# Kernel optimization log

Measured on AMD Instinct MI355X. Metric: run time of the kernel, lower is better.

The kernel has to match this reference:

```python
import jax, jax.numpy as jnp
import numpy as np

B, C, D, H, W = 4096, 64, 4, 4, 4
E, DIM = 16384, 4096  # num_embeddings, embedding_dim = C*D*H*W
COMMITMENT_COST = 0.25


def setup_inputs() -> dict:
    key = jax.random.key(0)
    k1, k2 = jax.random.split(key)
    inputs = jax.random.normal(k1, (B, C, D, H, W), dtype=jnp.float32)
    limit = 1.0 / E
    embed_w = jax.random.uniform(k2, (E, DIM), dtype=jnp.float32,
                                 minval=-limit, maxval=limit)
    return {"inputs": inputs, "embed_w": embed_w}


def reference(inputs, embed_w):
    sg = jax.lax.stop_gradient
    input_shape = inputs.shape
    flat = inputs.reshape(inputs.shape[0], -1)  # [B, DIM]
    distances = (jnp.sum(flat * flat, axis=1, keepdims=True)
                 + jnp.sum(embed_w * embed_w, axis=1)
                 - 2.0 * jnp.matmul(flat, embed_w.T))
    encoding_indices = jnp.argmin(distances, axis=1)  # [B]
    encodings = jax.nn.one_hot(encoding_indices, E, dtype=jnp.float32)  # [B, E]
    # gather nearest codebook vectors (same math as one_hot @ embed_w)
    quantized = embed_w[encoding_indices].reshape(input_shape)
    e_latent_loss = jnp.mean((sg(quantized) - inputs) ** 2)
    q_latent_loss = jnp.mean((quantized - sg(inputs)) ** 2)
    loss = q_latent_loss + COMMITMENT_COST * e_latent_loss
    # straight-through estimator
    quantized = inputs + sg(quantized - inputs)
    avg_probs = jnp.mean(encodings, axis=0)  # [E]
    perplexity = jnp.exp(-jnp.sum(avg_probs * jnp.log(avg_probs + 1e-10)))
    return loss, quantized, perplexity, encodings
```

## Files before the change

kernel.cpp:

```cpp
#include <hip/hip_runtime.h>

typedef unsigned long long u64;
typedef unsigned int u32;
typedef unsigned short u16;

typedef __attribute__((ext_vector_type(8))) short short8;
typedef __attribute__((ext_vector_type(4))) short short4v;
typedef __attribute__((ext_vector_type(4))) float floatx4;

static constexpr int BROWS = 4096;
static constexpr int ENUM_ = 16384;
static constexpr int KD    = 4096;
static constexpr int CANDMAX = 65536;
#define MARGIN 4e-4f


__device__ __forceinline__ u32 sortable(float d) {
  u32 u = __float_as_uint(d);
  return (u & 0x80000000u) ? ~u : (u | 0x80000000u);
}
__device__ __forceinline__ float unsortable(u32 k) {
  u32 u = (k & 0x80000000u) ? (k & 0x7fffffffu) : ~k;
  return __uint_as_float(u);
}

__device__ __forceinline__ u16 f2bf_rn(float f) {
  u32 u = __float_as_uint(f);
  u32 r = (u + 0x7fffu + ((u >> 16) & 1u)) >> 16;
  return (u16)r;
}
__device__ __forceinline__ float bf2f(u16 h) {
  return __uint_as_float((u32)h << 16);
}

__device__ __forceinline__ void gload_lds16(const void* g, void* l) {
  __builtin_amdgcn_global_load_lds((const __attribute__((address_space(1))) void*)g,
                                   (__attribute__((address_space(3))) void*)l,
                                   16, 0, 0);
}

__device__ __forceinline__ float blockReduceSumF(float v) {
  __shared__ float s[4];
  #pragma unroll
  for (int o = 32; o > 0; o >>= 1) v += __shfl_down(v, o);
  int lane = threadIdx.x & 63, wid = threadIdx.x >> 6;
  if (lane == 0) s[wid] = v;
  __syncthreads();
  float r = 0.f;
  if (threadIdx.x == 0) r = s[0] + s[1] + s[2] + s[3];
  return r;
}

__device__ __forceinline__ double blockReduceSumD(double v) {
  __shared__ double s[4];
  #pragma unroll
  for (int o = 32; o > 0; o >>= 1) v += __shfl_down(v, o);
  int lane = threadIdx.x & 63, wid = threadIdx.x >> 6;
  if (lane == 0) s[wid] = v;
  __syncthreads();
  double r = 0.0;
  if (threadIdx.x == 0) r = s[0] + s[1] + s[2] + s[3];
  return r;
}


__global__ __launch_bounds__(256) void split_hi(const float* __restrict__ src,
                                                u16* __restrict__ hi, int n8) {
  int t = blockIdx.x * 256 + threadIdx.x;
  if (t >= n8) return;
  const float4* s = (const float4*)src + (size_t)t * 2;
  float4 a = s[0], b = s[1];
  float v[8] = {a.x, a.y, a.z, a.w, b.x, b.y, b.z, b.w};
  short h[8];
  #pragma unroll
  for (int i = 0; i < 8; ++i) h[i] = (short)f2bf_rn(v[i]);
  *(short8*)(hi + (size_t)t * 8) = *(short8*)h;
}

__global__ __launch_bounds__(256) void split_w_e2(const float* __restrict__ w,
                                                  u16* __restrict__ hi,
                                                  float* __restrict__ e2) {
  int j = blockIdx.x;
  const float4* wr = (const float4*)(w + (size_t)j * KD);
  u16* hr = hi + (size_t)j * KD;
  float local = 0.f;
  #pragma unroll
  for (int t = 0; t < 4; ++t) {
    int e = threadIdx.x + t * 256;
    float4 v = wr[e];
    local += v.x * v.x + v.y * v.y + v.z * v.z + v.w * v.w;
    short h[4] = {(short)f2bf_rn(v.x), (short)f2bf_rn(v.y),
                  (short)f2bf_rn(v.z), (short)f2bf_rn(v.w)};
    *(short4v*)(hr + (size_t)e * 4) = *(short4v*)h;
  }
  float tot = blockReduceSumF(local);
  if (threadIdx.x == 0) e2[j] = tot;
}

__global__ __launch_bounds__(256) void split_kernel(const float* __restrict__ src,
                                                    u16* __restrict__ hi,
                                                    u16* __restrict__ lo, int n8) {
  int t = blockIdx.x * 256 + threadIdx.x;
  if (t >= n8) return;
  const float4* s = (const float4*)src + (size_t)t * 2;
  float4 a = s[0], b = s[1];
  float v[8] = {a.x, a.y, a.z, a.w, b.x, b.y, b.z, b.w};
  short h[8], l[8];
  #pragma unroll
  for (int i = 0; i < 8; ++i) {
    u16 hh = f2bf_rn(v[i]);
    h[i] = (short)hh;
    l[i] = (short)f2bf_rn(v[i] - bf2f(hh));
  }
  *(short8*)(hi + (size_t)t * 8) = *(short8*)h;
  *(short8*)(lo + (size_t)t * 8) = *(short8*)l;
}

__global__ __launch_bounds__(256) void e2_kernel(const float* __restrict__ w,
                                                 float* __restrict__ e2) {
  int j = blockIdx.x;
  const float4* wr = (const float4*)(w + (size_t)j * KD);
  float local = 0.f;
  #pragma unroll
  for (int t = 0; t < 4; ++t) {
    float4 v = wr[threadIdx.x + t * 256];
    local += v.x * v.x + v.y * v.y + v.z * v.z + v.w * v.w;
  }
  float tot = blockReduceSumF(local);
  if (threadIdx.x == 0) e2[j] = tot;
}

__global__ __launch_bounds__(512, 2)
void gemm_hi8(const u16* __restrict__ Ah, const u16* __restrict__ Bh,
              const float* __restrict__ e2, u16* __restrict__ dist,
              u64* __restrict__ best) {
  __shared__ char smem[131072];
  constexpr int NT = KD / 64;

  const u32 wg = blockIdx.x;
  const u32 swz = (wg & 7) * 128 + (wg >> 3);
  const int by = swz & 15;
  const int bx = swz >> 4;
  const int row0 = by * 256, col0 = bx * 256;

  const int t = threadIdx.x;
  const int lane = t & 63, wv = t >> 6;
  const int wr = wv >> 2, wc = wv & 3;
  const int quad = lane >> 4, lcol = lane & 15;

  const int m0 = t >> 2;
  const int g0 = (t & 3) ^ ((t >> 3) & 3);
  const size_t aG0 = (size_t)(row0 + m0) * KD + g0 * 8;
  const size_t bG0 = (size_t)(col0 + m0) * KD + g0 * 8;
  const size_t rowStep = (size_t)128 * KD;

  auto stage = [&](int tau, int k) {
    if (tau >= NT) return;
    char* base = smem + (tau & 1) * 65536 +
                 (k == 0 ? 0 : (k == 1 ? 32768 : (k == 2 ? 16384 : 49152)));
    size_t gofs = ((k == 0 || k == 2) ? aG0 : bG0) +
                  (size_t)tau * 64 + (k >= 2 ? 32 : 0);
    const u16* src = (k == 0 || k == 2) ? Ah : Bh;
    gload_lds16(src + gofs, base + t * 16);
    gload_lds16(src + gofs + rowStep, base + t * 16 + 8192);
  };

  stage(0, 0); stage(0, 1); stage(0, 2); stage(0, 3);
  stage(1, 0); stage(1, 1);
  asm volatile("s_waitcnt vmcnt(4)" ::: "memory");
  asm volatile("s_barrier" ::: "memory");

  floatx4 acc[8][4] = {};

  for (int tt = 0; tt < NT; ++tt) {
    char* buf = smem + (tt & 1) * 65536;
    short8 bf[4];
    #pragma unroll
    for (int c = 0; c < 4; ++c) {
      const int ks = c >> 1, mh = c & 1;
      const char* Ar = buf + ks * 16384;
      const char* Br = buf + 32768 + ks * 16384;

      short8 af[4];
      #pragma unroll
      for (int r = 0; r < 4; ++r) {
        int m = wr * 128 + mh * 64 + r * 16 + lcol;
        af[r] = *(const short8*)(Ar + m * 64 + ((quad ^ ((m >> 1) & 3)) << 4));
      }
      if (mh == 0) {
        #pragma unroll
        for (int n = 0; n < 4; ++n) {
          int mm = wc * 64 + n * 16 + lcol;
          bf[n] = *(const short8*)(Br + mm * 64 + ((quad ^ ((mm >> 1) & 3)) << 4));
        }
      }

      if (c == 0)      stage(tt + 1, 2);
      else if (c == 1) stage(tt + 1, 3);
      else if (c == 2) stage(tt + 2, 0);
      else             stage(tt + 2, 1);

      asm volatile("s_barrier" ::: "memory");
      __builtin_amdgcn_s_setprio(1);
      #pragma unroll
      for (int r = 0; r < 4; ++r)
        #pragma unroll
        for (int n = 0; n < 4; ++n)
          acc[mh * 4 + r][n] = __builtin_amdgcn_mfma_f32_16x16x32_bf16(
              af[r], bf[n], acc[mh * 4 + r][n], 0, 0, 0);
      __builtin_amdgcn_s_setprio(0);
      if (c == 3) asm volatile("s_waitcnt vmcnt(4)" ::: "memory");
      asm volatile("s_barrier" ::: "memory");
    }
  }

  float e2v[4];
  #pragma unroll
  for (int n = 0; n < 4; ++n) e2v[n] = e2[col0 + wc * 64 + n * 16 + lcol];

  #pragma unroll
  for (int fm = 0; fm < 8; ++fm) {
    #pragma unroll
    for (int i = 0; i < 4; ++i) {
      int grow = row0 + wr * 128 + fm * 16 + quad * 4 + i;
      u64 kmin = ~0ull;
      #pragma unroll
      for (int n = 0; n < 4; ++n) {
        int gcol = col0 + wc * 64 + n * 16 + lcol;
        float d = __fadd_rn(e2v[n], __fmul_rn(-2.0f, acc[fm][n][i]));
        dist[(size_t)grow * ENUM_ + gcol] = f2bf_rn(d);
        u64 key = ((u64)sortable(d) << 32) | (u32)gcol;
        kmin = key < kmin ? key : kmin;
      }
      #pragma unroll
      for (int msk = 1; msk < 16; msk <<= 1) {
        u64 o = __shfl_xor(kmin, msk);
        kmin = o < kmin ? o : kmin;
      }
      if (lcol == 0) atomicMin(&best[grow], kmin);
    }
  }
}

__global__ __launch_bounds__(256)
void scan_kernel(const u16* __restrict__ dist, const u64* __restrict__ best,
                 u64* __restrict__ cand, int* __restrict__ ccount) {
  const int n8 = BROWS * ENUM_ / 8;
  int step = gridDim.x * 256;
  for (int f = blockIdx.x * 256 + threadIdx.x; f < n8; f += step) {
    int i = f >> 11;
    float limit = unsortable((u32)(best[i] >> 32)) + MARGIN;
    short8 v = ((const short8*)dist)[f];
    #pragma unroll
    for (int e = 0; e < 8; ++e) {
      float d = bf2f((u16)v[e]);
      if (d <= limit) {
        int pos = atomicAdd(ccount, 1);
        if (pos < CANDMAX) cand[pos] = ((u64)(u32)i << 32) | (u32)(f * 8 + e - i * ENUM_);
      }
    }
  }
}

__global__ __launch_bounds__(256)
void refine_kernel(const float* __restrict__ x, const float* __restrict__ w,
                   const u64* __restrict__ cand, const int* __restrict__ ccount,
                   u64* __restrict__ best2) {
  int cnt = *ccount;
  if (cnt > CANDMAX) cnt = CANDMAX;
  for (int b = blockIdx.x; b < cnt; b += gridDim.x) {
    u64 cd = cand[b];
    int i = (int)(cd >> 32), j = (int)(cd & 0xffffffffu);
    const float4* xr = (const float4*)(x + (size_t)i * KD);
    const float4* wr = (const float4*)(w + (size_t)j * KD);
    double local = 0.0;
    #pragma unroll
    for (int t = 0; t < 4; ++t) {
      int e = threadIdx.x + t * 256;
      float4 xv = xr[e], wv = wr[e];
      local += (double)wv.x * ((double)wv.x - 2.0 * (double)xv.x)
             + (double)wv.y * ((double)wv.y - 2.0 * (double)xv.y)
             + (double)wv.z * ((double)wv.z - 2.0 * (double)xv.z)
             + (double)wv.w * ((double)wv.w - 2.0 * (double)xv.w);
    }
    double d = blockReduceSumD(local);
    if (threadIdx.x == 0) {
      u64 key = ((u64)sortable((float)d) << 32) | (u32)j;
      atomicMin(&best2[i], key);
    }
    __syncthreads();
  }
}

__global__ __launch_bounds__(256)
void gemm_argmin_mfma(const u16* __restrict__ Ah, const u16* __restrict__ Al,
                      const u16* __restrict__ Bh, const u16* __restrict__ Bl,
                      const float* __restrict__ e2, u64* __restrict__ best) {
  __shared__ char smem[32768];
  const int by = blockIdx.x, bx = blockIdx.y;
  const int row0 = by * 128, col0 = bx * 128;
  const int t = threadIdx.x;
  const int lane = t & 63, wv = t >> 6;
  const int wr = wv >> 1, wc = wv & 1;
  const int srow = t >> 2;
  const int schunk = (t & 3) ^ ((t >> 3) & 3);
  const size_t aoff0 = (size_t)(row0 + srow) * KD + schunk * 8;
  const size_t aoff1 = aoff0 + (size_t)64 * KD;
  const size_t boff0 = (size_t)(col0 + srow) * KD + schunk * 8;
  const size_t boff1 = boff0 + (size_t)64 * KD;
  char* sAh = smem; char* sAl = smem + 8192;
  char* sBh = smem + 16384; char* sBl = smem + 24576;
  const int d0 = t * 16, d1 = 4096 + t * 16;
  floatx4 acc[4][4] = {};
  for (int kk = 0; kk < KD; kk += 32) {
    __syncthreads();
    gload_lds16(Ah + aoff0 + kk, sAh + d0);
    gload_lds16(Ah + aoff1 + kk, sAh + d1);
    gload_lds16(Al + aoff0 + kk, sAl + d0);
    gload_lds16(Al + aoff1 + kk, sAl + d1);
    gload_lds16(Bh + boff0 + kk, sBh + d0);
    gload_lds16(Bh + boff1 + kk, sBh + d1);
    gload_lds16(Bl + boff0 + kk, sBl + d0);
    gload_lds16(Bl + boff1 + kk, sBl + d1);
    __syncthreads();
    short8 afh[4], afl[4];
    #pragma unroll
    for (int r = 0; r < 4; ++r) {
      int m = wr * 64 + r * 16 + (lane & 15);
      int off = m * 64 + (((lane >> 4) ^ ((m >> 1) & 3)) * 16);
      afh[r] = *(const short8*)(sAh + off);
      afl[r] = *(const short8*)(sAl + off);
    }
    #pragma unroll
    for (int c = 0; c < 4; ++c) {
      int m = wc * 64 + c * 16 + (lane & 15);
      int off = m * 64 + (((lane >> 4) ^ ((m >> 1) & 3)) * 16);
      short8 bfh = *(const short8*)(sBh + off);
      short8 bfl = *(const short8*)(sBl + off);
      #pragma unroll
      for (int r = 0; r < 4; ++r) {
        acc[r][c] = __builtin_amdgcn_mfma_f32_16x16x32_bf16(afh[r], bfh, acc[r][c], 0, 0, 0);
        acc[r][c] = __builtin_amdgcn_mfma_f32_16x16x32_bf16(afl[r], bfh, acc[r][c], 0, 0, 0);
        acc[r][c] = __builtin_amdgcn_mfma_f32_16x16x32_bf16(afh[r], bfl, acc[r][c], 0, 0, 0);
      }
    }
  }
  const int quad = lane >> 4, lcol = lane & 15;
  float e2v[4];
  #pragma unroll
  for (int c = 0; c < 4; ++c) e2v[c] = e2[col0 + wc * 64 + c * 16 + lcol];
  #pragma unroll
  for (int r = 0; r < 4; ++r) {
    #pragma unroll
    for (int i = 0; i < 4; ++i) {
      int grow = row0 + wr * 64 + r * 16 + quad * 4 + i;
      u64 kmin = ~0ull;
      #pragma unroll
      for (int c = 0; c < 4; ++c) {
        int gcol = col0 + wc * 64 + c * 16 + lcol;
        float d = __fadd_rn(e2v[c], __fmul_rn(-2.0f, acc[r][c][i]));
        u64 key = ((u64)sortable(d) << 32) | (u32)gcol;
        kmin = key < kmin ? key : kmin;
      }
      #pragma unroll
      for (int msk = 1; msk < 16; msk <<= 1) {
        u64 o = __shfl_xor(kmin, msk);
        kmin = o < kmin ? o : kmin;
      }
      if (lcol == 0) atomicMin(&best[grow], kmin);
    }
  }
}

__global__ __launch_bounds__(256)
void gemm_argmin(const float* __restrict__ A, const float* __restrict__ W,
                 const float* __restrict__ e2, u64* __restrict__ best) {
  __shared__ union {
    struct { float As[8][128]; float Bs[8][128]; } st;
    u64 red[128 * 16];
  } sm;
  const int by = blockIdx.x, bx = blockIdx.y;
  const int tid = threadIdx.x;
  const int tx = tid & 15, ty = tid >> 4;
  const int row0 = by * 128, col0 = bx * 128;
  const int lm = tid >> 1, lk = (tid & 1) * 4;
  const float* Ap = A + (size_t)(row0 + lm) * KD + lk;
  const float* Wp = W + (size_t)(col0 + lm) * KD + lk;
  float acc[8][8];
  #pragma unroll
  for (int r = 0; r < 8; ++r)
    #pragma unroll
    for (int c = 0; c < 8; ++c) acc[r][c] = 0.f;
  for (int kk = 0; kk < KD; kk += 8) {
    float4 av = *(const float4*)(Ap + kk);
    float4 bv = *(const float4*)(Wp + kk);
    __syncthreads();
    sm.st.As[lk + 0][lm] = av.x; sm.st.As[lk + 1][lm] = av.y;
    sm.st.As[lk + 2][lm] = av.z; sm.st.As[lk + 3][lm] = av.w;
    sm.st.Bs[lk + 0][lm] = bv.x; sm.st.Bs[lk + 1][lm] = bv.y;
    sm.st.Bs[lk + 2][lm] = bv.z; sm.st.Bs[lk + 3][lm] = bv.w;
    __syncthreads();
    #pragma unroll
    for (int k = 0; k < 8; ++k) {
      float a[8], b[8];
      *(float4*)&a[0] = *(const float4*)&sm.st.As[k][ty * 8];
      *(float4*)&a[4] = *(const float4*)&sm.st.As[k][ty * 8 + 4];
      *(float4*)&b[0] = *(const float4*)&sm.st.Bs[k][tx * 8];
      *(float4*)&b[4] = *(const float4*)&sm.st.Bs[k][tx * 8 + 4];
      #pragma unroll
      for (int r = 0; r < 8; ++r)
        #pragma unroll
        for (int c = 0; c < 8; ++c)
          acc[r][c] = fmaf(a[r], b[c], acc[r][c]);
    }
  }
  __syncthreads();
  float e2v[8];
  #pragma unroll
  for (int c = 0; c < 8; ++c) e2v[c] = e2[col0 + tx * 8 + c];
  #pragma unroll
  for (int r = 0; r < 8; ++r) {
    u64 bk = ~0ull;
    #pragma unroll
    for (int c = 0; c < 8; ++c) {
      int col = col0 + tx * 8 + c;
      float d = fmaf(-2.0f, acc[r][c], e2v[c]);
      u64 key = ((u64)sortable(d) << 32) | (u32)col;
      bk = key < bk ? key : bk;
    }
    sm.red[(ty * 8 + r) * 16 + tx] = bk;
  }
  __syncthreads();
  if (tid < 128) {
    u64 m = sm.red[tid * 16];
    #pragma unroll
    for (int t2 = 1; t2 < 16; ++t2) {
      u64 v = sm.red[tid * 16 + t2];
      m = v < m ? v : m;
    }
    atomicMin(&best[row0 + tid], m);
  }
}


__global__ __launch_bounds__(256) void scatter_kernel(const u64* __restrict__ best,
                                                      int* __restrict__ idx,
                                                      int* __restrict__ counts,
                                                      float* __restrict__ enc) {
  int i = blockIdx.x * 256 + threadIdx.x;
  u64 k = best[i];
  int j = (int)(k & 0xffffffffu);
  idx[i] = j;
  atomicAdd(&counts[j], 1);
  enc[(size_t)i * ENUM_ + j] = 1.0f;
}

__global__ __launch_bounds__(256) void gather_loss(const float* __restrict__ x,
                                                   const float* __restrict__ w,
                                                   const int* __restrict__ idx,
                                                   float* __restrict__ quant,
                                                   double* __restrict__ accum) {
  int i = blockIdx.x;
  int j = idx[i];
  const float4* wr = (const float4*)(w + (size_t)j * KD);
  const float4* xr = (const float4*)(x + (size_t)i * KD);
  float* qr = quant + (size_t)i * KD;
  double local = 0.0;
  #pragma unroll
  for (int t = 0; t < 4; ++t) {
    int e = threadIdx.x + t * 256;
    float4 wv = wr[e];
    float4 xv = xr[e];
    qr[4 * e + 0] = wv.x; qr[4 * e + 1] = wv.y;
    qr[4 * e + 2] = wv.z; qr[4 * e + 3] = wv.w;
    double d0 = (double)wv.x - (double)xv.x;
    double d1 = (double)wv.y - (double)xv.y;
    double d2 = (double)wv.z - (double)xv.z;
    double d3 = (double)wv.w - (double)xv.w;
    local += d0 * d0 + d1 * d1 + d2 * d2 + d3 * d3;
  }
  double tot = blockReduceSumD(local);
  if (threadIdx.x == 0) atomicAdd(accum, tot);
}

__global__ __launch_bounds__(256) void scalars_kernel(const int* __restrict__ counts,
                                                      const double* __restrict__ accum,
                                                      float* __restrict__ loss_out,
                                                      float* __restrict__ perp_out) {
  double local = 0.0;
  for (int j = threadIdx.x; j < ENUM_; j += 256) {
    double p = (double)counts[j] * (1.0 / 4096.0);
    local += p * log(p + 1e-10);
  }
  double s = blockReduceSumD(local);
  if (threadIdx.x == 0) {
    double mean = (*accum) * (1.0 / ((double)BROWS * (double)KD));
    loss_out[0] = (float)(1.25 * mean);
    perp_out[0] = (float)exp(-s);
  }
}


extern "C" void kernel_launch(void* const* d_in, const int* in_sizes, int n_in,
                              void* d_out, int out_size, void* d_ws, size_t ws_size,
                              hipStream_t stream) {
  const float* x = (const float*)d_in[0];
  const float* w = (const float*)d_in[1];
  float* out = (float*)d_out;

  char* ws = (char*)d_ws;
  u64* best     = (u64*)ws;
  u64* best2    = (u64*)(ws + 32768);
  int* idx      = (int*)(ws + 65536);
  int* counts   = (int*)(ws + 81920);
  double* accum = (double*)(ws + 147456);
  int* ccount   = (int*)(ws + 147464);
  float* e2     = (float*)(ws + 163840);
  u64* cand     = (u64*)(ws + 229376);
  u16* x_hi     = (u16*)(ws + 753664);
  u16* w_hi     = (u16*)(ws + 753664 + 33554432ull);
  char* regionR = ws + 753664 + 33554432ull + 134217728ull;
  u16* dist     = (u16*)regionR;
  u16* x_lo     = (u16*)regionR;
  u16* w_lo     = (u16*)(regionR + 33554432ull);
  const size_t NEED_FR = 168525824ull + 134217728ull;
  const size_t NEED_3T = 168525824ull + 167772160ull;

  float* loss_out = out;
  float* quant    = out + 1;
  float* perp_out = out + 16777217;
  float* enc      = out + 16777218;

  hipMemsetAsync(best, 0xFF, 65536, stream);
  hipMemsetAsync(counts, 0, 65536 + 16, stream);
  hipMemsetAsync(enc, 0, (size_t)BROWS * ENUM_ * sizeof(float), stream);

  if (ws_size >= NEED_FR) {
    split_hi<<<BROWS * KD / 8 / 256, 256, 0, stream>>>(x, x_hi, BROWS * KD / 8);
    split_w_e2<<<ENUM_, 256, 0, stream>>>(w, w_hi, e2);
    gemm_hi8<<<1024, 512, 0, stream>>>(x_hi, w_hi, e2, dist, best);
    scan_kernel<<<4096, 256, 0, stream>>>(dist, best, cand, ccount);
    refine_kernel<<<4096, 256, 0, stream>>>(x, w, cand, ccount, best2);
    scatter_kernel<<<BROWS / 256, 256, 0, stream>>>(best2, idx, counts, enc);
  } else if (ws_size >= NEED_3T) {
    e2_kernel<<<ENUM_, 256, 0, stream>>>(w, e2);
    split_kernel<<<BROWS * KD / 8 / 256, 256, 0, stream>>>(x, x_hi, x_lo, BROWS * KD / 8);
    split_kernel<<<ENUM_ * KD / 8 / 256, 256, 0, stream>>>(w, w_hi, w_lo, ENUM_ * KD / 8);
    gemm_argmin_mfma<<<dim3(32, 128), 256, 0, stream>>>(x_hi, x_lo, w_hi, w_lo, e2, best);
    scatter_kernel<<<BROWS / 256, 256, 0, stream>>>(best, idx, counts, enc);
  } else {
    e2_kernel<<<ENUM_, 256, 0, stream>>>(w, e2);
    gemm_argmin<<<dim3(32, 128), 256, 0, stream>>>(x, w, e2, best);
    scatter_kernel<<<BROWS / 256, 256, 0, stream>>>(best, idx, counts, enc);
  }
  gather_loss<<<BROWS, 256, 0, stream>>>(x, w, idx, quant, accum);
  scalars_kernel<<<1, 256, 0, stream>>>(counts, accum, loss_out, perp_out);
}
```

Before: 1.254 ms.

## Switch coarse distance GEMM from bf16 to per-row int8 quantized MFMA

Replaces the bf16 candidate GEMM with int8 per-row symmetric quantization of inputs and codebook, using the i32 16x16x64 int8 MFMA and rescaling by row scales in the epilogue. This halves operand bytes and doubles K per MFMA, cutting GEMM memory traffic and compute time. The refine stage still rescoring candidates in fp32 keeps exactness, and the margin is widened to absorb the larger quantization error, which may admit more candidates into the refine pass. Workspace layout shrinks accordingly.

```diff
diff --git a/kernel.cpp b/kernel.cpp
--- a/kernel.cpp
+++ b/kernel.cpp
@@ -7,12 +7,13 @@
 typedef __attribute__((ext_vector_type(8))) short short8;
 typedef __attribute__((ext_vector_type(4))) short short4v;
 typedef __attribute__((ext_vector_type(4))) float floatx4;
+typedef __attribute__((ext_vector_type(4))) int int4v;
 
 static constexpr int BROWS = 4096;
 static constexpr int ENUM_ = 16384;
 static constexpr int KD    = 4096;
 static constexpr int CANDMAX = 65536;
-#define MARGIN 4e-4f
+#define MARGIN 6e-4f
 
 
 __device__ __forceinline__ u32 sortable(float d) {
@@ -64,37 +65,82 @@
 }
 
 
-__global__ __launch_bounds__(256) void split_hi(const float* __restrict__ src,
-                                                u16* __restrict__ hi, int n8) {
-  int t = blockIdx.x * 256 + threadIdx.x;
-  if (t >= n8) return;
-  const float4* s = (const float4*)src + (size_t)t * 2;
-  float4 a = s[0], b = s[1];
-  float v[8] = {a.x, a.y, a.z, a.w, b.x, b.y, b.z, b.w};
-  short h[8];
-  #pragma unroll
-  for (int i = 0; i < 8; ++i) h[i] = (short)f2bf_rn(v[i]);
-  *(short8*)(hi + (size_t)t * 8) = *(short8*)h;
-}
-
-__global__ __launch_bounds__(256) void split_w_e2(const float* __restrict__ w,
-                                                  u16* __restrict__ hi,
+__global__ __launch_bounds__(256) void quant_x(const float* __restrict__ x,
+                                               signed char* __restrict__ xq,
+                                               float* __restrict__ sx) {
+  int i = blockIdx.x;
+  const float4* xr = (const float4*)(x + (size_t)i * KD);
+  float4 v[4];
+  float mx = 0.f;
+  #pragma unroll
+  for (int t = 0; t < 4; ++t) {
+    v[t] = xr[threadIdx.x + t * 256];
+    mx = fmaxf(mx, fmaxf(fmaxf(fabsf(v[t].x), fabsf(v[t].y)),
+                         fmaxf(fabsf(v[t].z), fabsf(v[t].w))));
+  }
+  #pragma unroll
+  for (int o = 32; o > 0; o >>= 1) mx = fmaxf(mx, __shfl_down(mx, o));
+  __shared__ float red[4];
+  int lane = threadIdx.x & 63, wid = threadIdx.x >> 6;
+  if (lane == 0) red[wid] = mx;
+  __syncthreads();
+  float m = fmaxf(fmaxf(red[0], red[1]), fmaxf(red[2], red[3]));
+  float inv = m > 0.f ? 127.f / m : 0.f;
+  u32* qr = (u32*)(xq + (size_t)i * KD);
+  #pragma unroll
+  for (int t = 0; t < 4; ++t) {
+    int e = threadIdx.x + t * 256;
+    int q0 = __float2int_rn(v[t].x * inv);
+    int q1 = __float2int_rn(v[t].y * inv);
+    int q2 = __float2int_rn(v[t].z * inv);
+    int q3 = __float2int_rn(v[t].w * inv);
+    qr[e] = ((u32)(q0 & 0xff)) | ((u32)(q1 & 0xff) << 8) |
+            ((u32)(q2 & 0xff) << 16) | ((u32)(q3 & 0xff) << 24);
+  }
+  if (threadIdx.x == 0) sx[i] = m * (1.f / 127.f);
+}
+
+__global__ __launch_bounds__(256) void quant_w_e2(const float* __restrict__ w,
+                                                  signed char* __restrict__ wq,
+                                                  float* __restrict__ sw,
                                                   float* __restrict__ e2) {
   int j = blockIdx.x;
   const float4* wr = (const float4*)(w + (size_t)j * KD);
-  u16* hr = hi + (size_t)j * KD;
-  float local = 0.f;
+  float4 v[4];
+  float mx = 0.f, s2 = 0.f;
+  #pragma unroll
+  for (int t = 0; t < 4; ++t) {
+    v[t] = wr[threadIdx.x + t * 256];
+    s2 += v[t].x * v[t].x + v[t].y * v[t].y + v[t].z * v[t].z + v[t].w * v[t].w;
+    mx = fmaxf(mx, fmaxf(fmaxf(fabsf(v[t].x), fabsf(v[t].y)),
+                         fmaxf(fabsf(v[t].z), fabsf(v[t].w))));
+  }
+  #pragma unroll
+  for (int o = 32; o > 0; o >>= 1) {
+    s2 += __shfl_down(s2, o);
+    mx = fmaxf(mx, __shfl_down(mx, o));
+  }
+  __shared__ float redS[4], redM[4];
+  int lane = threadIdx.x & 63, wid = threadIdx.x >> 6;
+  if (lane == 0) { redS[wid] = s2; redM[wid] = mx; }
+  __syncthreads();
+  float m = fmaxf(fmaxf(redM[0], redM[1]), fmaxf(redM[2], redM[3]));
+  float inv = m > 0.f ? 127.f / m : 0.f;
+  u32* qr = (u32*)(wq + (size_t)j * KD);
   #pragma unroll
   for (int t = 0; t < 4; ++t) {
     int e = threadIdx.x + t * 256;
-    float4 v = wr[e];
-    local += v.x * v.x + v.y * v.y + v.z * v.z + v.w * v.w;
-    short h[4] = {(short)f2bf_rn(v.x), (short)f2bf_rn(v.y),
-                  (short)f2bf_rn(v.z), (short)f2bf_rn(v.w)};
-    *(short4v*)(hr + (size_t)e * 4) = *(short4v*)h;
-  }
-  float tot = blockReduceSumF(local);
-  if (threadIdx.x == 0) e2[j] = tot;
+    int q0 = __float2int_rn(v[t].x * inv);
+    int q1 = __float2int_rn(v[t].y * inv);
+    int q2 = __float2int_rn(v[t].z * inv);
+    int q3 = __float2int_rn(v[t].w * inv);
+    qr[e] = ((u32)(q0 & 0xff)) | ((u32)(q1 & 0xff) << 8) |
+            ((u32)(q2 & 0xff) << 16) | ((u32)(q3 & 0xff) << 24);
+  }
+  if (threadIdx.x == 0) {
+    sw[j] = m * (1.f / 127.f);
+    e2[j] = redS[0] + redS[1] + redS[2] + redS[3];
+  }
 }
 
 __global__ __launch_bounds__(256) void split_kernel(const float* __restrict__ src,
@@ -131,11 +177,12 @@
 }
 
 __global__ __launch_bounds__(512, 2)
-void gemm_hi8(const u16* __restrict__ Ah, const u16* __restrict__ Bh,
-              const float* __restrict__ e2, u16* __restrict__ dist,
-              u64* __restrict__ best) {
+void gemm_i8(const signed char* __restrict__ Aq, const signed char* __restrict__ Bq,
+             const float* __restrict__ sx, const float* __restrict__ sw,
+             const float* __restrict__ e2, u16* __restrict__ dist,
+             u64* __restrict__ best) {
   __shared__ char smem[131072];
-  constexpr int NT = KD / 64;
+  constexpr int NT = KD / 128;
 
   const u32 wg = blockIdx.x;
   const u32 swz = (wg & 7) * 128 + (wg >> 3);
@@ -150,8 +197,8 @@
 
   const int m0 = t >> 2;
   const int g0 = (t & 3) ^ ((t >> 3) & 3);
-  const size_t aG0 = (size_t)(row0 + m0) * KD + g0 * 8;
-  const size_t bG0 = (size_t)(col0 + m0) * KD + g0 * 8;
+  const size_t aG0 = (size_t)(row0 + m0) * KD + g0 * 16;
+  const size_t bG0 = (size_t)(col0 + m0) * KD + g0 * 16;
   const size_t rowStep = (size_t)128 * KD;
 
   auto stage = [&](int tau, int k) {
@@ -159,8 +206,8 @@
     char* base = smem + (tau & 1) * 65536 +
                  (k == 0 ? 0 : (k == 1 ? 32768 : (k == 2 ? 16384 : 49152)));
     size_t gofs = ((k == 0 || k == 2) ? aG0 : bG0) +
-                  (size_t)tau * 64 + (k >= 2 ? 32 : 0);
-    const u16* src = (k == 0 || k == 2) ? Ah : Bh;
+                  (size_t)tau * 128 + (k >= 2 ? 64 : 0);
+    const signed char* src = (k == 0 || k == 2) ? Aq : Bq;
     gload_lds16(src + gofs, base + t * 16);
     gload_lds16(src + gofs + rowStep, base + t * 16 + 8192);
   };
@@ -170,28 +217,28 @@
   asm volatile("s_waitcnt vmcnt(4)" ::: "memory");
   asm volatile("s_barrier" ::: "memory");
 
-  floatx4 acc[8][4] = {};
+  int4v acc[8][4] = {};
 
   for (int tt = 0; tt < NT; ++tt) {
     char* buf = smem + (tt & 1) * 65536;
-    short8 bf[4];
+    int4v bf[4];
     #pragma unroll
     for (int c = 0; c < 4; ++c) {
       const int ks = c >> 1, mh = c & 1;
       const char* Ar = buf + ks * 16384;
       const char* Br = buf + 32768 + ks * 16384;
 
-      short8 af[4];
+      int4v af[4];
       #pragma unroll
       for (int r = 0; r < 4; ++r) {
         int m = wr * 128 + mh * 64 + r * 16 + lcol;
-        af[r] = *(const short8*)(Ar + m * 64 + ((quad ^ ((m >> 1) & 3)) << 4));
+        af[r] = *(const int4v*)(Ar + m * 64 + ((quad ^ ((m >> 1) & 3)) << 4));
       }
       if (mh == 0) {
         #pragma unroll
         for (int n = 0; n < 4; ++n) {
           int mm = wc * 64 + n * 16 + lcol;
-          bf[n] = *(const short8*)(Br + mm * 64 + ((quad ^ ((mm >> 1) & 3)) << 4));
+          bf[n] = *(const int4v*)(Br + mm * 64 + ((quad ^ ((mm >> 1) & 3)) << 4));
         }
       }
 
@@ -206,7 +253,7 @@
       for (int r = 0; r < 4; ++r)
         #pragma unroll
         for (int n = 0; n < 4; ++n)
-          acc[mh * 4 + r][n] = __builtin_amdgcn_mfma_f32_16x16x32_bf16(
+          acc[mh * 4 + r][n] = __builtin_amdgcn_mfma_i32_16x16x64_i8(
               af[r], bf[n], acc[mh * 4 + r][n], 0, 0, 0);
       __builtin_amdgcn_s_setprio(0);
       if (c == 3) asm volatile("s_waitcnt vmcnt(4)" ::: "memory");
@@ -214,20 +261,26 @@
     }
   }
 
-  float e2v[4];
-  #pragma unroll
-  for (int n = 0; n < 4; ++n) e2v[n] = e2[col0 + wc * 64 + n * 16 + lcol];
+  float e2v[4], sc2[4];
+  #pragma unroll
+  for (int n = 0; n < 4; ++n) {
+    int gc = col0 + wc * 64 + n * 16 + lcol;
+    e2v[n] = e2[gc];
+    sc2[n] = -2.0f * sw[gc];
+  }
 
   #pragma unroll
   for (int fm = 0; fm < 8; ++fm) {
     #pragma unroll
     for (int i = 0; i < 4; ++i) {
       int grow = row0 + wr * 128 + fm * 16 + quad * 4 + i;
+      float sxr = sx[grow];
       u64 kmin = ~0ull;
       #pragma unroll
       for (int n = 0; n < 4; ++n) {
         int gcol = col0 + wc * 64 + n * 16 + lcol;
-        float d = __fadd_rn(e2v[n], __fmul_rn(-2.0f, acc[fm][n][i]));
+        float d = __fadd_rn(e2v[n],
+                            __fmul_rn(sc2[n] * sxr, (float)acc[fm][n][i]));
         dist[(size_t)grow * ENUM_ + gcol] = f2bf_rn(d);
         u64 key = ((u64)sortable(d) << 32) | (u32)gcol;
         kmin = key < kmin ? key : kmin;
@@ -517,13 +570,19 @@
   int* ccount   = (int*)(ws + 147464);
   float* e2     = (float*)(ws + 163840);
   u64* cand     = (u64*)(ws + 229376);
+
+  signed char* x_q = (signed char*)(ws + 753664);
+  signed char* w_q = (signed char*)(ws + 17530880);
+  float* s_x    = (float*)(ws + 84639744);
+  float* s_w    = (float*)(ws + 84656128);
+  u16* dist     = (u16*)(ws + 84721664);
+  const size_t NEED_FR = 84721664ull + 134217728ull;
+
   u16* x_hi     = (u16*)(ws + 753664);
   u16* w_hi     = (u16*)(ws + 753664 + 33554432ull);
-  char* regionR = ws + 753664 + 33554432ull + 134217728ull;
-  u16* dist     = (u16*)regionR;
-  u16* x_lo     = (u16*)regionR;
-  u16* w_lo     = (u16*)(regionR + 33554432ull);
-  const size_t NEED_FR = 168525824ull + 134217728ull;
+  char* regionO = ws + 753664 + 33554432ull + 134217728ull;
+  u16* x_lo     = (u16*)regionO;
+  u16* w_lo     = (u16*)(regionO + 33554432ull);
   const size_t NEED_3T = 168525824ull + 167772160ull;
 
   float* loss_out = out;
@@ -536,9 +595,9 @@
   hipMemsetAsync(enc, 0, (size_t)BROWS * ENUM_ * sizeof(float), stream);
 
   if (ws_size >= NEED_FR) {
-    split_hi<<<BROWS * KD / 8 / 256, 256, 0, stream>>>(x, x_hi, BROWS * KD / 8);
-    split_w_e2<<<ENUM_, 256, 0, stream>>>(w, w_hi, e2);
-    gemm_hi8<<<1024, 512, 0, stream>>>(x_hi, w_hi, e2, dist, best);
+    quant_x<<<BROWS, 256, 0, stream>>>(x, x_q, s_x);
+    quant_w_e2<<<ENUM_, 256, 0, stream>>>(w, w_q, s_w, e2);
+    gemm_i8<<<1024, 512, 0, stream>>>(x_q, w_q, s_x, s_w, e2, dist, best);
     scan_kernel<<<4096, 256, 0, stream>>>(dist, best, cand, ccount);
     refine_kernel<<<4096, 256, 0, stream>>>(x, w, cand, ccount, best2);
     scatter_kernel<<<BROWS / 256, 256, 0, stream>>>(best2, idx, counts, enc);
```

Result: faster. 1.065 ms (-15.0%).
